# Performance work log

Hardware: AMD Instinct MI355X
Metric: run time of the kernel (lower is better)

## Reference

```python
import jax, jax.numpy as jnp
import numpy as np

HS = 512; L = 4; T = 128; M = 2048; FF = 2048; NH = 4; DH = HS // NH
STDV = 1.0 / float(np.sqrt(HS))


def setup_inputs() -> dict:
    key = jax.random.key(0)
    ks = iter(jax.random.split(key, 32))

    def u(shape):
        return jax.random.uniform(next(ks), shape, jnp.float32, -STDV, STDV)

    return {
        "x": jax.random.normal(next(ks), (1, T, HS), jnp.float32),
        "historical_states": jax.random.normal(next(ks), (M, L, HS), jnp.float32),
        "Wx": u((L, 3, HS, HS)), "bx": u((L, 3, HS)),
        "Wh": u((L, 3, HS, HS)), "bh": u((L, 3, HS)),
        "sa_Win": u((L, 3 * HS, HS)), "sa_bin": u((L, 3 * HS)),
        "sa_Wo": u((L, HS, HS)), "sa_bo": u((L, HS)),
        "ca_Win": u((L, 3 * HS, HS)), "ca_bin": u((L, 3 * HS)),
        "ca_Wo": u((L, HS, HS)), "ca_bo": u((L, HS)),
        "ff_W1": u((L, FF, HS)), "ff_b1": u((L, FF)),
        "ff_W2": u((L, HS, FF)), "ff_b2": u((L, HS)),
        "ln_g": u((L, 3, HS)), "ln_b": u((L, 3, HS)),
    }


def _layer_norm(v, g, b):
    m = v.mean(-1, keepdims=True)
    var = ((v - m) ** 2).mean(-1, keepdims=True)
    return (v - m) / jnp.sqrt(var + 1e-5) * g + b


def _forward(x, historical_states, Wx, bx, Wh, bh, sa_Win, sa_bin, sa_Wo, sa_bo,
             ca_Win, ca_bin, ca_Wo, ca_bo, ff_W1, ff_b1, ff_W2, ff_b2, ln_g, ln_b):
    n_layers, _, hs, _ = Wx.shape
    # Cross-attn K/V over the static historical memory are time-invariant: precompute once.
    Wk = ca_Win[:, hs:2 * hs, :]; bk = ca_bin[:, hs:2 * hs]
    Wv = ca_Win[:, 2 * hs:, :]; bv = ca_bin[:, 2 * hs:]
    K = (jnp.einsum('mle,lfe->lmf', historical_states, Wk) + bk[:, None, :]).reshape(n_layers, -1, NH, DH)
    V = (jnp.einsum('mle,lfe->lmf', historical_states, Wv) + bv[:, None, :]).reshape(n_layers, -1, NH, DH)
    scale = 1.0 / jnp.sqrt(jnp.asarray(DH, x.dtype))

    def decoder(i, f):
        # post-norm TransformerDecoderLayer, tgt length 1, eval mode (no dropout).
        # Self-attn over a single position: softmax of one logit == 1 -> out = Wo @ (Wv_self f + bv_self) + bo.
        v_sa = sa_Win[i, 2 * hs:] @ f + sa_bin[i, 2 * hs:]
        sa = sa_Wo[i] @ v_sa + sa_bo[i]
        x1 = _layer_norm(f + sa, ln_g[i, 0], ln_b[i, 0])
        q = (ca_Win[i, :hs] @ x1 + ca_bin[i, :hs]).reshape(NH, DH)
        att = jax.nn.softmax(jnp.einsum('hd,mhd->hm', q, K[i]) * scale, axis=-1)
        ctx = jnp.einsum('hm,mhd->hd', att, V[i]).reshape(hs)
        x2 = _layer_norm(x1 + ca_Wo[i] @ ctx + ca_bo[i], ln_g[i, 1], ln_b[i, 1])
        ff = ff_W2[i] @ jax.nn.relu(ff_W1[i] @ x2 + ff_b1[i]) + ff_b2[i]
        return _layer_norm(x2 + ff, ln_g[i, 2], ln_b[i, 2])

    def step(carry, x_t):
        h_prev, c_prev = carry  # (L, HS) each; batch is structurally 1
        xin = x_t
        h_new = []; c_new = []
        for i in range(n_layers):
            z = (jnp.einsum('gij,j->gi', Wx[i], xin) + bx[i]
                 + jnp.einsum('gij,j->gi', Wh[i], h_prev[i]) + bh[i])  # (3, HS)
            i_t = jax.nn.sigmoid(z[0]); f0 = jax.nn.sigmoid(z[1]); g_t = jnp.tanh(z[2])
            f_t = jax.nn.sigmoid(c_prev[i] - decoder(i, f0))
            c_i = f_t * c_prev[i] + i_t * g_t
            xin = jnp.tanh(c_i)
            h_new.append(xin); c_new.append(c_i)
        h = jnp.stack(h_new); c = jnp.stack(c_new)
        return (h, c), h[-1]

    h0 = jnp.zeros((n_layers, hs), x.dtype)
    c0 = jnp.zeros((n_layers, hs), x.dtype)
    (h_T, c_T), hidden = jax.lax.scan(step, (h0, c0), x[0])  # hidden: (T, HS)
    return hidden[None], h_T[:, None, :], c_T[:, None, :]


def reference(x, historical_states, Wx, bx, Wh, bh, sa_Win, sa_bin, sa_Wo, sa_bo,
              ca_Win, ca_bin, ca_Wo, ca_bo, ff_W1, ff_b1, ff_W2, ff_b2, ln_g, ln_b):
    return _forward(x, historical_states, Wx, bx, Wh, bh, sa_Win, sa_bin, sa_Wo, sa_bo,
                    ca_Win, ca_bin, ca_Wo, ca_bo, ff_W1, ff_b1, ff_W2, ff_b2, ln_g, ln_b)
```

## Files before the change

### kernel.cpp

```cpp
#include <hip/hip_runtime.h>

#define HS   512
#define LNUM 4
#define TT   128
#define MMEM 2048
#define FFD  2048
#define NB   256
#define NT   512
#define INV512 (1.0f/512.0f)
#define QSCALE 0.08838834764831845f

typedef unsigned short ushortt;

constexpr size_t KHALF = (size_t)LNUM*MMEM*HS/2;
constexpr size_t HHALF = (size_t)LNUM*HS*HS/2;
constexpr size_t FHALF = (size_t)LNUM*FFD*HS/2;
constexpr size_t OFF_KBF    = 0;
constexpr size_t OFF_VBF    = OFF_KBF    + KHALF;
constexpr size_t OFF_WCOMBBF= OFF_VBF    + KHALF;
constexpr size_t OFF_WQP    = OFF_WCOMBBF+ HHALF;
constexpr size_t OFF_W2P    = OFF_WQP    + HHALF;
constexpr size_t OFF_FFW1BF = OFF_W2P    + FHALF;
constexpr size_t OFF_CAWOBF = OFF_FFW1BF + FHALF;
constexpr size_t OFF_CSA    = OFF_CAWOBF + HHALF;
constexpr size_t OFF_SQ     = OFF_CSA    + (size_t)LNUM*HS;
constexpr size_t OFF_CBQ    = OFF_SQ     + (size_t)LNUM*HS;
constexpr size_t OFF_STATE = OFF_CBQ   + (size_t)LNUM*HS;
constexpr size_t OFF_H     = OFF_STATE;
constexpr size_t OFF_C     = OFF_H     + 2*LNUM*HS;
constexpr size_t OFF_XING  = OFF_C     + 2*LNUM*HS;
constexpr size_t OFF_Z1    = OFF_XING  + HS;
constexpr size_t OFF_Z02   = OFF_Z1    + HS;
constexpr size_t OFF_T2G   = OFF_Z02   + 2*HS;
constexpr size_t OFF_YP    = OFF_T2G   + HS;
constexpr size_t OFF_Y2P   = OFF_YP    + 4*HS;
constexpr size_t OFF_CTXP  = OFF_Y2P   + 8*HS;
constexpr size_t OFF_DENS  = OFF_CTXP  + 8*HS;
constexpr size_t OFF_S1S   = OFF_DENS  + 128;
constexpr size_t OFF_S2S   = OFF_S1S   + 64;
constexpr size_t OFF_J1    = OFF_S2S   + 64;
constexpr size_t OFF_J2    = OFF_J1    + 65*32;
constexpr size_t OFF_FLAGS = OFF_J2    + 128*32;
constexpr size_t WS_TOTAL  = OFF_FLAGS + (size_t)NB*32;

__device__ __forceinline__ float wred(float v) {
#pragma unroll
  for (int m = 32; m; m >>= 1) v += __shfl_xor(v, m);
  return v;
}
__device__ __forceinline__ float sigm(float x) { return 1.0f/(1.0f+__expf(-x)); }
__device__ __forceinline__ ushortt f2bf(float f) {
  unsigned u = __float_as_uint(f);
  return (ushortt)((u + 0x7fffu + ((u >> 16) & 1u)) >> 16);
}
__device__ __forceinline__ float bflo(unsigned v){ return __uint_as_float(v << 16); }
__device__ __forceinline__ float bfhi(unsigned v){ return __uint_as_float(v & 0xffff0000u); }
__device__ __forceinline__ void ld8bfp(const ushortt* p, unsigned* d) {
  uint4 v = *(const uint4*)p;
  d[0] = v.x; d[1] = v.y; d[2] = v.z; d[3] = v.w;
}
__device__ __forceinline__ void ld8f(const float* p, float* d) {
  float4 a = *(const float4*)p, b = *(const float4*)(p + 4);
  d[0]=a.x; d[1]=a.y; d[2]=a.z; d[3]=a.w; d[4]=b.x; d[5]=b.y; d[6]=b.z; d[7]=b.w;
}

__device__ __forceinline__ float ald(const float* p) {
  return __hip_atomic_load(p, __ATOMIC_RELAXED, __HIP_MEMORY_SCOPE_AGENT);
}
__device__ __forceinline__ void ast(float* p, float v) {
  __hip_atomic_store(p, v, __ATOMIC_RELAXED, __HIP_MEMORY_SCOPE_AGENT);
}
__device__ __forceinline__ unsigned aldu(const unsigned* p) {
  return __hip_atomic_load(p, __ATOMIC_RELAXED, __HIP_MEMORY_SCOPE_AGENT);
}
__device__ __forceinline__ void astu(unsigned* p, unsigned v) {
  __hip_atomic_store(p, v, __ATOMIC_RELAXED, __HIP_MEMORY_SCOPE_AGENT);
}

template <class F>
__device__ __forceinline__ void barrier_pf(unsigned* flags, unsigned g, F&& pf) {
  asm volatile("s_waitcnt vmcnt(0)" ::: "memory");
  __syncthreads();
  if (threadIdx.x == 0) astu(flags + (size_t)blockIdx.x*32, g);
  pf();
  if (threadIdx.x < NB) {
    const unsigned* f = flags + (size_t)threadIdx.x*32;
    while ((int)(aldu(f) - g) < 0) __builtin_amdgcn_s_sleep(2);
  }
  __syncthreads();
}
__device__ __forceinline__ void jflag(unsigned* J, int id, unsigned val) {
  asm volatile("s_waitcnt vmcnt(0)" ::: "memory");
  __syncthreads();
  if (threadIdx.x == 0) astu(J + (size_t)id*32, val);
}
template <class F>
__device__ __forceinline__ void jwait_pf(unsigned* J, int n, unsigned val, F&& pf) {
  pf();
  if (threadIdx.x < n) {
    const unsigned* f = J + (size_t)threadIdx.x*32;
    while ((int)(aldu(f) - val) < 0) __builtin_amdgcn_s_sleep(1);
  }
  __syncthreads();
}
__device__ __forceinline__ void slotred32(const float* slots, float* sh, int o,
                                          int w, int lane) {
  if (w == 0) {
    float a = (lane < 32) ? ald(slots + lane*2) : ald(slots + (lane-32)*2 + 1);
#pragma unroll
    for (int m = 16; m; m >>= 1) a += __shfl_xor(a, m);
    if (lane == 0)  sh[o]   = a;
    if (lane == 32) sh[o+1] = a;
  }
}


__global__ __launch_bounds__(256) void kv_gemm(
    const float* __restrict__ hist, const float* __restrict__ caWin,
    const float* __restrict__ caBin, ushortt* __restrict__ out, int koff, int vt) {
  __shared__ float As[16][64];
  __shared__ float Bs[16][64];
  const int l = blockIdx.z, m0 = blockIdx.x*64, f0 = blockIdx.y*64;
  const int tid = threadIdx.x, tm = tid >> 4, tf = tid & 15;
  float acc[4][4] = {};
  for (int e0 = 0; e0 < HS; e0 += 16) {
#pragma unroll
    for (int it = 0; it < 4; ++it) {
      int idx = tid + it*256, k = idx & 15, mm = idx >> 4;
      As[k][mm] = hist[((size_t)(m0+mm)*LNUM + l)*HS + e0 + k];
      Bs[k][mm] = caWin[((size_t)l*(3*HS) + koff + f0 + mm)*HS + e0 + k];
    }
    __syncthreads();
#pragma unroll
    for (int k = 0; k < 16; ++k) {
      float a[4], b[4];
#pragma unroll
      for (int xx = 0; xx < 4; ++xx) { a[xx] = As[k][tm*4+xx]; b[xx] = Bs[k][tf*4+xx]; }
#pragma unroll
      for (int xx = 0; xx < 4; ++xx)
#pragma unroll
        for (int y = 0; y < 4; ++y) acc[xx][y] += a[xx]*b[y];
    }
    __syncthreads();
  }
#pragma unroll
  for (int xx = 0; xx < 4; ++xx)
#pragma unroll
    for (int y = 0; y < 4; ++y) {
      int m = m0 + tm*4 + xx, f = f0 + tf*4 + y;
      ushortt v = f2bf(acc[xx][y] + caBin[l*(3*HS) + koff + f]);
      if (vt) out[(size_t)l*MMEM*HS + (size_t)f*MMEM + m] = v;
      else    out[((size_t)l*MMEM + m)*HS + f] = v;
    }
}

__global__ __launch_bounds__(256) void wcomb_gemm(
    const float* __restrict__ saWo, const float* __restrict__ saWin,
    ushortt* __restrict__ wcomb) {
  __shared__ float As[16][64];
  __shared__ float Bs[16][64];
  const int l = blockIdx.z, f0 = blockIdx.x*64, j0 = blockIdx.y*64;
  const int tid = threadIdx.x, tm = tid >> 4, tf = tid & 15;
  float acc[4][4] = {};
  for (int e0 = 0; e0 < HS; e0 += 16) {
#pragma unroll
    for (int it = 0; it < 4; ++it) {
      int idx = tid + it*256;
      { int k = idx & 15, ff = idx >> 4;
        As[k][ff] = saWo[((size_t)l*HS + f0+ff)*HS + e0 + k]; }
      { int jj = idx & 63, k = idx >> 6;
        Bs[k][jj] = saWin[((size_t)l*(3*HS) + 2*HS + e0 + k)*HS + j0 + jj]; }
    }
    __syncthreads();
#pragma unroll
    for (int k = 0; k < 16; ++k) {
      float a[4], b[4];
#pragma unroll
      for (int xx = 0; xx < 4; ++xx) { a[xx] = As[k][tm*4+xx]; b[xx] = Bs[k][tf*4+xx]; }
#pragma unroll
      for (int xx = 0; xx < 4; ++xx)
#pragma unroll
        for (int y = 0; y < 4; ++y) acc[xx][y] += a[xx]*b[y];
    }
    __syncthreads();
  }
#pragma unroll
  for (int xx = 0; xx < 4; ++xx)
#pragma unroll
    for (int y = 0; y < 4; ++y)
      wcomb[(size_t)l*HS*HS + (size_t)(f0+tm*4+xx)*HS + (j0+tf*4+y)] = f2bf(acc[xx][y]);
}

__global__ __launch_bounds__(256) void pack_wq(
    const float* __restrict__ caWin, const float* __restrict__ lnG,
    ushortt* __restrict__ wqp) {
  const int b = blockIdx.x, l = blockIdx.y;
  for (int idx = threadIdx.x; idx < 512*16; idx += 256) {
    int f = idx >> 4, r = idx & 15, j = b*16 + r;
    wqp[(((size_t)l*32 + b)*512 + f)*16 + r] =
        f2bf(caWin[((size_t)l*3*HS + f)*HS + j] * lnG[l*3*HS + j]);
  }
}

__global__ __launch_bounds__(256) void pack_w2(
    const float* __restrict__ ffW2, ushortt* __restrict__ w2p) {
  const int bid = blockIdx.x, l = blockIdx.y;
  for (int idx = threadIdx.x; idx < 512*8; idx += 256) {
    int f = idx >> 3, r = idx & 7;
    w2p[(((size_t)l*NB + bid)*512 + f)*8 + r] =
        f2bf(ffW2[((size_t)l*HS + f)*FFD + bid*8 + r]);
  }
}

__global__ __launch_bounds__(256) void bf16_copy(
    const float* __restrict__ in, ushortt* __restrict__ out, size_t n) {
  for (size_t i = (size_t)blockIdx.x*256 + threadIdx.x; i < n; i += (size_t)gridDim.x*256)
    out[i] = f2bf(in[i]);
}

__global__ __launch_bounds__(256) void csa_kernel(
    const float* __restrict__ saWo, const float* __restrict__ sabin,
    const float* __restrict__ sabo, float* __restrict__ csa) {
  const int w = threadIdx.x >> 6, lane = threadIdx.x & 63;
  const int row = blockIdx.x*4 + w;
  const int l = row >> 9, f = row & 511;
  float acc = 0;
#pragma unroll
  for (int k = 0; k < 8; ++k) {
    int e = lane + 64*k;
    acc += saWo[((size_t)l*HS + f)*HS + e] * sabin[l*(3*HS) + 2*HS + e];
  }
  acc = wred(acc);
  if (lane == 0) csa[row] = acc + sabo[l*HS + f];
}

__global__ __launch_bounds__(256) void sqcbq_kernel(
    const float* __restrict__ caWin, const float* __restrict__ caBin,
    const float* __restrict__ lnG, const float* __restrict__ lnB,
    float* __restrict__ sq, float* __restrict__ cbq) {
  const int w = threadIdx.x >> 6, lane = threadIdx.x & 63;
  const int row = blockIdx.x*4 + w;
  const int l = row >> 9, f = row & 511;
  float a1 = 0, a2 = 0;
#pragma unroll
  for (int k = 0; k < 8; ++k) {
    int e = lane + 64*k;
    float wv = caWin[((size_t)l*(3*HS) + f)*HS + e];
    a1 += wv * lnG[l*(3*HS) + e];
    a2 += wv * lnB[l*(3*HS) + e];
  }
  a1 = wred(a1); a2 = wred(a2);
  if (lane == 0) { sq[row] = a1; cbq[row] = a2 + caBin[l*(3*HS) + f]; }
}


__global__ __launch_bounds__(NT, 1) void seq_kernel(
    const float* __restrict__ x,
    const float* __restrict__ Wx,  const float* __restrict__ bx,
    const float* __restrict__ Wh,  const float* __restrict__ bh,
    const float* __restrict__ caBo,
    const float* __restrict__ ffB1,
    const float* __restrict__ ffB2,
    const float* __restrict__ lnG,  const float* __restrict__ lnB,
    float* __restrict__ ws, float* __restrict__ out) {
  const ushortt* Kb    = (const ushortt*)(ws + OFF_KBF);
  const ushortt* Vt    = (const ushortt*)(ws + OFF_VBF);
  const ushortt* Wcomb = (const ushortt*)(ws + OFF_WCOMBBF);
  const ushortt* WQP   = (const ushortt*)(ws + OFF_WQP);
  const ushortt* W2P   = (const ushortt*)(ws + OFF_W2P);
  const ushortt* F1b   = (const ushortt*)(ws + OFF_FFW1BF);
  const ushortt* CaWob = (const ushortt*)(ws + OFF_CAWOBF);
  const float* csag  = ws + OFF_CSA;
  const float* sqg   = ws + OFF_SQ;
  const float* cbqg  = ws + OFF_CBQ;
  float* hG    = ws + OFF_H;
  float* cG    = ws + OFF_C;
  float* xing  = ws + OFF_XING;
  float* z1g   = ws + OFF_Z1;
  float* z02g  = ws + OFF_Z02;
  float* t2g   = ws + OFF_T2G;
  float* Yp    = ws + OFF_YP;
  float* Y2p   = ws + OFF_Y2P;
  float* ctxP  = ws + OFF_CTXP;
  float* denS  = ws + OFF_DENS;
  float* s1s   = ws + OFF_S1S;
  float* s2s   = ws + OFF_S2S;
  unsigned* J1     = (unsigned*)(ws + OFF_J1);
  unsigned* J2     = (unsigned*)(ws + OFF_J2);
  unsigned* bflags = (unsigned*)(ws + OFF_FLAGS);

  __shared__ float sh_xin[HS], sh_h[HS], sh_vec[HS], sh_aux[HS];
  __shared__ float sh_q[128], sh_p[64], sh_t1[16];
  __shared__ float sh_red[24], sh_den[4];

  const int bid = blockIdx.x, tid = threadIdx.x;
  const int w = tid >> 6, lane = tid & 63;
  unsigned gen = 1;

  float    pZx[8],  pZh[8];
  float    pZx2[8], pZh2[8];
  unsigned pWc[2][4], pWq[8];
  unsigned pK[2][4],  pV[8];
  unsigned pCa[2][4];
  unsigned pF1[4], pW2[4];

  auto pfH1 = [&](int l) {
    if (bid < 64) {
      const size_t ro = (((size_t)l*3 + 1)*HS + bid*8 + w)*HS + lane*8;
      ld8f(Wx + ro, pZx);
      ld8f(Wh + ro, pZh);
    }
  };
  auto pfH2 = [&](int l) {
    if (bid < 32) {
#pragma unroll
      for (int rr = 0; rr < 2; ++rr)
        ld8bfp(Wcomb + ((size_t)l*HS + bid*16 + w*2 + rr)*HS + lane*8, pWc[rr]);
      const ushortt* q = WQP + (((size_t)l*32 + bid)*512 + tid)*16;
      ld8bfp(q,     pWq);
      ld8bfp(q + 8, pWq + 4);
    }
  };
  auto pfH3 = [&](int l) {
    if (bid >= 32 && bid < 160) {
      const int b2 = bid - 32, h = b2 >> 5, ms = b2 & 31;
#pragma unroll
      for (int rr = 0; rr < 2; ++rr)
        ld8bfp(Kb + ((size_t)l*MMEM + ms*64 + w*8 + (lane>>4) + 4*rr)*HS
                  + h*128 + (lane & 15)*8, pK[rr]);
      const ushortt* vp = Vt + (size_t)l*MMEM*HS
                        + ((size_t)h*128 + (tid & 127))*MMEM + ms*64 + (tid >> 7)*16;
      ld8bfp(vp,     pV);
      ld8bfp(vp + 8, pV + 4);
    }
  };
  auto pfZ = [&](int l) {
    if (bid < 32 || bid >= 160) {
      const int zb = (bid < 32) ? bid : bid - 128;
      const int rowid = zb*8 + w;
      const int g = (rowid < 512) ? 0 : 2;
      const int f = rowid & 511;
      const size_t ro = (((size_t)l*3 + g)*HS + f)*HS + lane*8;
      ld8f(Wx + ro, pZx2);
      ld8f(Wh + ro, pZh2);
    }
  };
  auto pfH4 = [&](int l) {
    if (bid < 32) {
#pragma unroll
      for (int rr = 0; rr < 2; ++rr)
        ld8bfp(CaWob + ((size_t)l*HS + bid*16 + w*2 + rr)*HS + lane*8, pCa[rr]);
    }
  };
  auto pfH5 = [&](int l) {
    ld8bfp(F1b + ((size_t)l*FFD + bid*8 + w)*HS + lane*8, pF1);
    ld8bfp(W2P + (((size_t)l*NB + bid)*512 + tid)*8, pW2);
  };

  auto do_update = [&](int ip, int parp, float& xn, float& cn) {
    const int j = tid;
    float t2v = ald(t2g + j);
    float z0  = ald(z02g + j);
    float z2  = ald(z02g + HS + j);
    float y2 = 0;
    {
      float yv[8];
#pragma unroll
      for (int p = 0; p < 8; ++p) yv[p] = ald(Y2p + (size_t)p*HS + j);
#pragma unroll
      for (int p = 0; p < 8; ++p) y2 += yv[p];
    }
    slotred32(s2s, sh_red, 16, w, lane);
    __syncthreads();
    float m2 = sh_red[16]*INV512;
    float r2 = rsqrtf(sh_red[17]*INV512 - m2*m2 + 1e-5f);
    float x2 = (t2v-m2)*r2*lnG[(ip*3+1)*HS+j] + lnB[(ip*3+1)*HS+j];
    float t3 = x2 + y2 + ffB2[ip*HS + j];
    float s_ = t3, q_ = t3*t3;
#pragma unroll
    for (int m = 32; m; m >>= 1) { s_ += __shfl_xor(s_, m); q_ += __shfl_xor(q_, m); }
    if (lane == 0) { sh_red[w] = s_; sh_red[8+w] = q_; }
    __syncthreads();
    if (tid == 0) {
      float a = 0, b = 0;
#pragma unroll
      for (int k = 0; k < 8; ++k) { a += sh_red[k]; b += sh_red[8+k]; }
      sh_red[0] = a; sh_red[1] = b;
    }
    __syncthreads();
    float m3 = sh_red[0]*INV512;
    float r3 = rsqrtf(sh_red[1]*INV512 - m3*m3 + 1e-5f);
    float d  = (t3-m3)*r3*lnG[(ip*3+2)*HS+j] + lnB[(ip*3+2)*HS+j];
    float cp = ald(cG + (parp*LNUM + ip)*HS + j);
    float ft = sigm(cp - d);
    float it = sigm(z0);
    float gt = tanhf(z2);
    cn = ft*cp + it*gt;
    xn = tanhf(cn);
  };

  pfH1(0); pfH2(0); pfH3(0);

  for (int s = 0; s < TT*LNUM; ++s) {
    const int t = s >> 2, i = s & 3;
    const int par = t & 1;
    const unsigned jv = (unsigned)(s + 1);
    if (bid < 64) {
      float xn = 0.f, cn = 0.f;
      if (s > 0) {
        const int ip = (s-1) & 3, tp = (s-1) >> 2, parp = tp & 1;
        if (bid == 0 || i > 0) {
          do_update(ip, parp, xn, cn);
          if (bid == 0) {
            ast(hG + ((parp^1)*LNUM + ip)*HS + tid, xn);
            ast(cG + ((parp^1)*LNUM + ip)*HS + tid, cn);
            if (ip == 3) out[tp*HS + tid] = xn;
          }
        }
      }
      float xv = (i == 0) ? x[t*HS + tid] : xn;
      sh_xin[tid] = xv;
      sh_h[tid]   = ald(hG + (par*LNUM + i)*HS + tid);
      if (bid == 0) ast(xing + tid, xv);
      __syncthreads();
      const int f = bid*8 + w;
      float acc = 0;
#pragma unroll
      for (int m = 0; m < 8; ++m)
        acc += pZx[m]*sh_xin[lane*8+m] + pZh[m]*sh_h[lane*8+m];
      acc = wred(acc);
      if (lane == 0) ast(z1g + f, acc + bx[(i*3+1)*HS + f] + bh[(i*3+1)*HS + f]);
      jflag(J1, bid, jv);
    } else if (bid == 64) {
#pragma unroll
      for (int p = 0; p < 4; ++p) ast(Yp + (size_t)p*HS + tid, 0.f);
      jflag(J1, 64, jv);
    } else if (bid == 65) {
#pragma unroll
      for (int p = 0; p < 8; ++p) ast(ctxP + (size_t)p*HS + tid, 0.f);
    } else if (bid == 66) {
      jwait_pf(J1, 65, jv, [&]{});
#pragma unroll
      for (int p = 0; p < 8; ++p) ast(Y2p + (size_t)p*HS + tid, 0.f);
    }
    if (bid < 32) {
      jwait_pf(J1, 65, jv, [&]{});
      sh_vec[tid] = sigm(ald(z1g + tid));
      __syncthreads();
#pragma unroll
      for (int rr = 0; rr < 2; ++rr) {
        const int r = w*2 + rr, j = bid*16 + r;
        float acc = 0;
#pragma unroll
        for (int k = 0; k < 4; ++k) {
          unsigned pw = pWc[rr][k];
          acc += bflo(pw)*sh_vec[lane*8 + 2*k] + bfhi(pw)*sh_vec[lane*8 + 2*k + 1];
        }
        acc = wred(acc);
        if (lane == 0) {
          float t1v = sh_vec[j] + acc + csag[i*HS + j];
          sh_t1[r]  = t1v;
          sh_aux[r] = t1v;
        }
      }
      __syncthreads();
      {
        float yl = 0;
#pragma unroll
        for (int q = 0; q < 8; ++q) {
          unsigned pw = pWq[q];
          yl += sh_aux[2*q]*bflo(pw) + sh_aux[2*q+1]*bfhi(pw);
        }
        atomicAdd(&Yp[(size_t)(bid & 3)*HS + tid], yl);
      }
      if (w == 0 && lane < 16) {
        float v = sh_aux[lane], s_ = v, q_ = v*v;
#pragma unroll
        for (int m = 8; m; m >>= 1) { s_ += __shfl_xor(s_, m); q_ += __shfl_xor(q_, m); }
        if (lane == 0) { ast(s1s + bid*2, s_); ast(s1s + bid*2 + 1, q_); }
      }
    }
    barrier_pf(bflags, gen, [&]{ pfZ(i); pfH4(i); pfH5(i); });
    if (bid >= 32 && bid < 160) {
      const int b2 = bid - 32, h = b2 >> 5;
      slotred32(s1s, sh_red, 18, w, lane);
      __syncthreads();
      if (tid < 128) {
        float m1 = sh_red[18]*INV512;
        float r1 = rsqrtf(sh_red[19]*INV512 - m1*m1 + 1e-5f);
        int f = h*128 + tid;
        float Ysum = 0;
#pragma unroll
        for (int p = 0; p < 4; ++p) Ysum += ald(Yp + (size_t)p*HS + f);
        sh_q[tid] = r1*(Ysum - m1*sqg[i*HS + f]) + cbqg[i*HS + f];
      }
      __syncthreads();
#pragma unroll
      for (int rr = 0; rr < 2; ++rr) {
        float sc = 0;
#pragma unroll
        for (int k = 0; k < 4; ++k) {
          unsigned pw = pK[rr][k];
          sc += bflo(pw)*sh_q[(lane & 15)*8 + 2*k] + bfhi(pw)*sh_q[(lane & 15)*8 + 2*k + 1];
        }
#pragma unroll
        for (int msk = 8; msk; msk >>= 1) sc += __shfl_xor(sc, msk);
        if ((lane & 15) == 0) sh_p[w*8 + (lane >> 4) + 4*rr] = __expf(sc * QSCALE);
      }
      __syncthreads();
      {
        const int d = tid & 127, mg = tid >> 7;
        float acc = 0;
#pragma unroll
        for (int q = 0; q < 8; ++q) {
          unsigned pw = pV[q];
          acc += sh_p[mg*16 + 2*q]*bflo(pw) + sh_p[mg*16 + 2*q + 1]*bfhi(pw);
        }
        atomicAdd(&ctxP[(size_t)((b2 & 1)*4 + mg)*HS + h*128 + d], acc);
      }
      if (w == 0) {
        float v = wred(sh_p[lane]);
        if (lane == 0) ast(denS + h*32 + (b2 & 31), v);
      }
      jflag(J2, b2, jv);
    } else {
      const int zb = (bid < 32) ? bid : bid - 128;
      if (bid >= 160) {
        sh_xin[tid] = ald(xing + tid);
        sh_h[tid]   = ald(hG + (par*LNUM + i)*HS + tid);
      }
      __syncthreads();
      const int rowid = zb*8 + w;
      const int g = (rowid < 512) ? 0 : 2;
      const int f = rowid & 511;
      float acc = 0;
#pragma unroll
      for (int m = 0; m < 8; ++m)
        acc += pZx2[m]*sh_xin[lane*8+m] + pZh2[m]*sh_h[lane*8+m];
      acc = wred(acc);
      if (lane == 0) ast(z02g + (g ? HS : 0) + f, acc + bx[(i*3+g)*HS + f] + bh[(i*3+g)*HS + f]);
      if (bid < 32) {
        jwait_pf(J2, 128, jv, [&]{});
        slotred32(s1s, sh_red, 18, w, lane);
        if (w >= 4) {
          float v = (lane < 32) ? ald(denS + (w-4)*32 + lane) : 0.f;
#pragma unroll
          for (int m = 16; m; m >>= 1) v += __shfl_xor(v, m);
          if (lane == 0) sh_den[w-4] = v;
        }
        __syncthreads();
        const float m1 = sh_red[18]*INV512;
        const float r1 = rsqrtf(sh_red[19]*INV512 - m1*m1 + 1e-5f);
        {
          float c = 0;
#pragma unroll
          for (int p = 0; p < 8; ++p) c += ald(ctxP + (size_t)p*HS + tid);
          sh_vec[tid] = c / sh_den[tid >> 7];
        }
        __syncthreads();
#pragma unroll
        for (int rr = 0; rr < 2; ++rr) {
          const int r = w*2 + rr, j = bid*16 + r;
          float a2 = 0;
#pragma unroll
          for (int k = 0; k < 4; ++k) {
            unsigned pw = pCa[rr][k];
            a2 += bflo(pw)*sh_vec[lane*8 + 2*k] + bfhi(pw)*sh_vec[lane*8 + 2*k + 1];
          }
          a2 = wred(a2);
          if (lane == 0) {
            float x1 = (sh_t1[r]-m1)*r1*lnG[(i*3)*HS + j] + lnB[(i*3)*HS + j];
            float t2v = x1 + a2 + caBo[i*HS + j];
            ast(t2g + j, t2v);
            sh_aux[r] = t2v;
          }
        }
        __syncthreads();
        if (w == 0 && lane < 16) {
          float v = sh_aux[lane], s_ = v, q_ = v*v;
#pragma unroll
          for (int m = 8; m; m >>= 1) { s_ += __shfl_xor(s_, m); q_ += __shfl_xor(q_, m); }
          if (lane == 0) { ast(s2s + bid*2, s_); ast(s2s + bid*2 + 1, q_); }
        }
      }
    }
    barrier_pf(bflags, gen+1, [&]{ const int nl = (s+1) & 3; pfH1(nl); pfH2(nl); pfH3(nl); });
    {
      slotred32(s2s, sh_red, 16, w, lane);
      __syncthreads();
      const float m2 = sh_red[16]*INV512;
      const float r2 = rsqrtf(sh_red[17]*INV512 - m2*m2 + 1e-5f);
      sh_vec[tid] = (ald(t2g + tid)-m2)*r2*lnG[(i*3+1)*HS + tid] + lnB[(i*3+1)*HS + tid];
      __syncthreads();
      const int kk = bid*8 + w;
      float acc = 0;
#pragma unroll
      for (int k = 0; k < 4; ++k) {
        unsigned pw = pF1[k];
        acc += bflo(pw)*sh_vec[lane*8 + 2*k] + bfhi(pw)*sh_vec[lane*8 + 2*k + 1];
      }
      acc = wred(acc);
      if (lane == 0) sh_aux[w] = fmaxf(acc + ffB1[i*FFD + kk], 0.f);
      __syncthreads();
      float yl = 0;
#pragma unroll
      for (int q = 0; q < 4; ++q) {
        unsigned pw = pW2[q];
        yl += sh_aux[2*q]*bflo(pw) + sh_aux[2*q+1]*bfhi(pw);
      }
      atomicAdd(&Y2p[(size_t)(bid & 7)*HS + tid], yl);
    }
    barrier_pf(bflags, gen+2, [&]{});
    gen += 3;
  }

  if (bid == 0) {
    float xn, cn;
    do_update(3, 1, xn, cn);
    out[127*HS + tid] = xn;
    out[TT*HS + 3*HS + tid] = xn;
    out[TT*HS + LNUM*HS + 3*HS + tid] = cn;
#pragma unroll
    for (int ii = 0; ii < 3; ++ii) {
      out[TT*HS + ii*HS + tid]            = ald(hG + (0*LNUM + ii)*HS + tid);
      out[TT*HS + LNUM*HS + ii*HS + tid]  = ald(cG + (0*LNUM + ii)*HS + tid);
    }
  }
}

extern "C" void kernel_launch(void* const* d_in, const int* in_sizes, int n_in,
                              void* d_out, int out_size, void* d_ws, size_t ws_size,
                              hipStream_t stream) {
  const float* x      = (const float*)d_in[0];
  const float* hist   = (const float*)d_in[1];
  const float* Wx     = (const float*)d_in[2];
  const float* bx     = (const float*)d_in[3];
  const float* Wh     = (const float*)d_in[4];
  const float* bh     = (const float*)d_in[5];
  const float* saWin  = (const float*)d_in[6];
  const float* saBin  = (const float*)d_in[7];
  const float* saWo   = (const float*)d_in[8];
  const float* saBo   = (const float*)d_in[9];
  const float* caWin  = (const float*)d_in[10];
  const float* caBin  = (const float*)d_in[11];
  const float* caWo   = (const float*)d_in[12];
  const float* caBo   = (const float*)d_in[13];
  const float* ffW1   = (const float*)d_in[14];
  const float* ffB1   = (const float*)d_in[15];
  const float* ffW2   = (const float*)d_in[16];
  const float* ffB2   = (const float*)d_in[17];
  const float* lnG    = (const float*)d_in[18];
  const float* lnB    = (const float*)d_in[19];
  float* ws  = (float*)d_ws;
  float* out = (float*)d_out;

  hipMemsetAsync((char*)d_ws + OFF_STATE*sizeof(float), 0,
                 (WS_TOTAL - OFF_STATE)*sizeof(float), stream);

  kv_gemm<<<dim3(MMEM/64, HS/64, LNUM), 256, 0, stream>>>(
      hist, caWin, caBin, (ushortt*)(ws + OFF_KBF), HS, 0);
  kv_gemm<<<dim3(MMEM/64, HS/64, LNUM), 256, 0, stream>>>(
      hist, caWin, caBin, (ushortt*)(ws + OFF_VBF), 2*HS, 1);
  wcomb_gemm<<<dim3(HS/64, HS/64, LNUM), 256, 0, stream>>>(
      saWo, saWin, (ushortt*)(ws + OFF_WCOMBBF));
  csa_kernel<<<(LNUM*HS)/4, 256, 0, stream>>>(saWo, saBin, saBo, ws + OFF_CSA);
  pack_wq<<<dim3(32, LNUM), 256, 0, stream>>>(caWin, lnG, (ushortt*)(ws + OFF_WQP));
  sqcbq_kernel<<<(LNUM*HS)/4, 256, 0, stream>>>(caWin, caBin, lnG, lnB, ws + OFF_SQ, ws + OFF_CBQ);
  pack_w2<<<dim3(NB, LNUM), 256, 0, stream>>>(ffW2, (ushortt*)(ws + OFF_W2P));
  bf16_copy<<<2048, 256, 0, stream>>>(ffW1, (ushortt*)(ws + OFF_FFW1BF), (size_t)LNUM*FFD*HS);
  bf16_copy<<<1024, 256, 0, stream>>>(caWo, (ushortt*)(ws + OFF_CAWOBF), (size_t)LNUM*HS*HS);

  seq_kernel<<<NB, NT, 0, stream>>>(x, Wx, bx, Wh, bh, caBo,
                                    ffB1, ffB2, lnG, lnB, ws, out);
}
```

Baseline: 11.09 ms.

## Move z0/z2 gate GEMV to idle blocks, bf16 LSTM weights, drop atomics

Wx and Wh are converted to bf16 in the workspace so the LSTM gate GEMVs read half the bytes. The z0/z2 gate rows move from blocks 0-31 and 160-255 onto blocks 64-191, which wait on a new per-step xing flag, and z02 is double-buffered by step parity. Attention partials (Yp, ctxP) now go to per-block slots with no atomics, and readers reduce them in shared memory. The FFN accumulator is spread over 64 slots and the H2/H3 prefetches move to the last barrier. The aim is to take the gate GEMV off the critical cross-attention chain and cut atomic contention, at the cost of more slot reads and a new flag protocol.

New measurement: 21.63 ms. +95.2%, slower.

```diff
diff --git a/kernel.cpp b/kernel.cpp
--- a/kernel.cpp
+++ b/kernel.cpp
@@ -15,6 +15,7 @@
 constexpr size_t KHALF = (size_t)LNUM*MMEM*HS/2;
 constexpr size_t HHALF = (size_t)LNUM*HS*HS/2;
 constexpr size_t FHALF = (size_t)LNUM*FFD*HS/2;
+constexpr size_t GHALF = (size_t)LNUM*3*HS*HS/2;
 constexpr size_t OFF_KBF    = 0;
 constexpr size_t OFF_VBF    = OFF_KBF    + KHALF;
 constexpr size_t OFF_WCOMBBF= OFF_VBF    + KHALF;
@@ -22,7 +23,9 @@
 constexpr size_t OFF_W2P    = OFF_WQP    + HHALF;
 constexpr size_t OFF_FFW1BF = OFF_W2P    + FHALF;
 constexpr size_t OFF_CAWOBF = OFF_FFW1BF + FHALF;
-constexpr size_t OFF_CSA    = OFF_CAWOBF + HHALF;
+constexpr size_t OFF_WXBF   = OFF_CAWOBF + HHALF;
+constexpr size_t OFF_WHBF   = OFF_WXBF   + GHALF;
+constexpr size_t OFF_CSA    = OFF_WHBF   + GHALF;
 constexpr size_t OFF_SQ     = OFF_CSA    + (size_t)LNUM*HS;
 constexpr size_t OFF_CBQ    = OFF_SQ     + (size_t)LNUM*HS;
 constexpr size_t OFF_STATE = OFF_CBQ   + (size_t)LNUM*HS;
@@ -31,16 +34,17 @@
 constexpr size_t OFF_XING  = OFF_C     + 2*LNUM*HS;
 constexpr size_t OFF_Z1    = OFF_XING  + HS;
 constexpr size_t OFF_Z02   = OFF_Z1    + HS;
-constexpr size_t OFF_T2G   = OFF_Z02   + 2*HS;
+constexpr size_t OFF_T2G   = OFF_Z02   + 2*2*HS;
 constexpr size_t OFF_YP    = OFF_T2G   + HS;
-constexpr size_t OFF_Y2P   = OFF_YP    + 4*HS;
-constexpr size_t OFF_CTXP  = OFF_Y2P   + 8*HS;
-constexpr size_t OFF_DENS  = OFF_CTXP  + 8*HS;
+constexpr size_t OFF_Y2P   = OFF_YP    + 32*HS;
+constexpr size_t OFF_CTXP  = OFF_Y2P   + 64*HS;
+constexpr size_t OFF_DENS  = OFF_CTXP  + 128*128;
 constexpr size_t OFF_S1S   = OFF_DENS  + 128;
 constexpr size_t OFF_S2S   = OFF_S1S   + 64;
 constexpr size_t OFF_J1    = OFF_S2S   + 64;
-constexpr size_t OFF_J2    = OFF_J1    + 65*32;
-constexpr size_t OFF_FLAGS = OFF_J2    + 128*32;
+constexpr size_t OFF_J2    = OFF_J1    + 64*32;
+constexpr size_t OFF_XFL   = OFF_J2    + 128*32;
+constexpr size_t OFF_FLAGS = OFF_XFL   + 4*32;
 constexpr size_t WS_TOTAL  = OFF_FLAGS + (size_t)NB*32;
 
 __device__ __forceinline__ float wred(float v) {
@@ -58,10 +62,6 @@
 __device__ __forceinline__ void ld8bfp(const ushortt* p, unsigned* d) {
   uint4 v = *(const uint4*)p;
   d[0] = v.x; d[1] = v.y; d[2] = v.z; d[3] = v.w;
-}
-__device__ __forceinline__ void ld8f(const float* p, float* d) {
-  float4 a = *(const float4*)p, b = *(const float4*)(p + 4);
-  d[0]=a.x; d[1]=a.y; d[2]=a.z; d[3]=a.w; d[4]=b.x; d[5]=b.y; d[6]=b.z; d[7]=b.w;
 }
 
 __device__ __forceinline__ float ald(const float* p) {
@@ -94,9 +94,7 @@
   __syncthreads();
   if (threadIdx.x == 0) astu(J + (size_t)id*32, val);
 }
-template <class F>
-__device__ __forceinline__ void jwait_pf(unsigned* J, int n, unsigned val, F&& pf) {
-  pf();
+__device__ __forceinline__ void jwait(unsigned* J, int n, unsigned val) {
   if (threadIdx.x < n) {
     const unsigned* f = J + (size_t)threadIdx.x*32;
     while ((int)(aldu(f) - val) < 0) __builtin_amdgcn_s_sleep(1);
@@ -256,8 +254,7 @@
 
 __global__ __launch_bounds__(NT, 1) void seq_kernel(
     const float* __restrict__ x,
-    const float* __restrict__ Wx,  const float* __restrict__ bx,
-    const float* __restrict__ Wh,  const float* __restrict__ bh,
+    const float* __restrict__ bx, const float* __restrict__ bh,
     const float* __restrict__ caBo,
     const float* __restrict__ ffB1,
     const float* __restrict__ ffB2,
@@ -270,6 +267,8 @@
   const ushortt* W2P   = (const ushortt*)(ws + OFF_W2P);
   const ushortt* F1b   = (const ushortt*)(ws + OFF_FFW1BF);
   const ushortt* CaWob = (const ushortt*)(ws + OFF_CAWOBF);
+  const ushortt* WXb   = (const ushortt*)(ws + OFF_WXBF);
+  const ushortt* WHb   = (const ushortt*)(ws + OFF_WHBF);
   const float* csag  = ws + OFF_CSA;
   const float* sqg   = ws + OFF_SQ;
   const float* cbqg  = ws + OFF_CBQ;
@@ -287,6 +286,7 @@
   float* s2s   = ws + OFF_S2S;
   unsigned* J1     = (unsigned*)(ws + OFF_J1);
   unsigned* J2     = (unsigned*)(ws + OFF_J2);
+  unsigned* xfl    = (unsigned*)(ws + OFF_XFL);
   unsigned* bflags = (unsigned*)(ws + OFF_FLAGS);
 
   __shared__ float sh_xin[HS], sh_h[HS], sh_vec[HS], sh_aux[HS];
@@ -295,10 +295,11 @@
 
   const int bid = blockIdx.x, tid = threadIdx.x;
   const int w = tid >> 6, lane = tid & 63;
+  const int g4 = tid >> 7, dd = tid & 127;
   unsigned gen = 1;
 
-  float    pZx[8],  pZh[8];
-  float    pZx2[8], pZh2[8];
+  unsigned pZx[4],  pZh[4];
+  unsigned pZx2[4], pZh2[4];
   unsigned pWc[2][4], pWq[8];
   unsigned pK[2][4],  pV[8];
   unsigned pCa[2][4];
@@ -307,8 +308,17 @@
   auto pfH1 = [&](int l) {
     if (bid < 64) {
       const size_t ro = (((size_t)l*3 + 1)*HS + bid*8 + w)*HS + lane*8;
-      ld8f(Wx + ro, pZx);
-      ld8f(Wh + ro, pZh);
+      ld8bfp(WXb + ro, pZx);
+      ld8bfp(WHb + ro, pZh);
+    }
+  };
+  auto pfZ02 = [&](int l) {
+    if (bid >= 64 && bid < 192) {
+      const int zb = bid - 64, rowid = zb*8 + w;
+      const int g = (rowid < 512) ? 0 : 2, f = rowid & 511;
+      const size_t ro = (((size_t)l*3 + g)*HS + f)*HS + lane*8;
+      ld8bfp(WXb + ro, pZx2);
+      ld8bfp(WHb + ro, pZh2);
     }
   };
   auto pfH2 = [&](int l) {
@@ -329,20 +339,9 @@
         ld8bfp(Kb + ((size_t)l*MMEM + ms*64 + w*8 + (lane>>4) + 4*rr)*HS
                   + h*128 + (lane & 15)*8, pK[rr]);
       const ushortt* vp = Vt + (size_t)l*MMEM*HS
-                        + ((size_t)h*128 + (tid & 127))*MMEM + ms*64 + (tid >> 7)*16;
+                        + ((size_t)h*128 + dd)*MMEM + ms*64 + g4*16;
       ld8bfp(vp,     pV);
       ld8bfp(vp + 8, pV + 4);
-    }
-  };
-  auto pfZ = [&](int l) {
-    if (bid < 32 || bid >= 160) {
-      const int zb = (bid < 32) ? bid : bid - 128;
-      const int rowid = zb*8 + w;
-      const int g = (rowid < 512) ? 0 : 2;
-      const int f = rowid & 511;
-      const size_t ro = (((size_t)l*3 + g)*HS + f)*HS + lane*8;
-      ld8f(Wx + ro, pZx2);
-      ld8f(Wh + ro, pZh2);
     }
   };
   auto pfH4 = [&](int l) {
@@ -357,18 +356,21 @@
     ld8bfp(W2P + (((size_t)l*NB + bid)*512 + tid)*8, pW2);
   };
 
-  auto do_update = [&](int ip, int parp, float& xn, float& cn) {
+  auto do_update = [&](int ip, int parp, int pz, float& xn, float& cn) {
     const int j = tid;
     float t2v = ald(t2g + j);
-    float z0  = ald(z02g + j);
-    float z2  = ald(z02g + HS + j);
+    float z0  = ald(z02g + pz*1024 + j);
+    float z2  = ald(z02g + pz*1024 + HS + j);
     float y2 = 0;
     {
-      float yv[8];
-#pragma unroll
-      for (int p = 0; p < 8; ++p) yv[p] = ald(Y2p + (size_t)p*HS + j);
-#pragma unroll
-      for (int p = 0; p < 8; ++p) y2 += yv[p];
+      float yv[16];
+#pragma unroll
+      for (int c = 0; c < 64; c += 16) {
+#pragma unroll
+        for (int p = 0; p < 16; ++p) yv[p] = ald(Y2p + (size_t)(c+p)*HS + j);
+#pragma unroll
+        for (int p = 0; p < 16; ++p) y2 += yv[p];
+      }
     }
     slotred32(s2s, sh_red, 16, w, lane);
     __syncthreads();
@@ -399,18 +401,19 @@
     xn = tanhf(cn);
   };
 
-  pfH1(0); pfH2(0); pfH3(0);
+  pfH1(0); pfZ02(0); pfH2(0); pfH3(0);
 
   for (int s = 0; s < TT*LNUM; ++s) {
     const int t = s >> 2, i = s & 3;
     const int par = t & 1;
+    const int pz = s & 1;
     const unsigned jv = (unsigned)(s + 1);
     if (bid < 64) {
       float xn = 0.f, cn = 0.f;
       if (s > 0) {
         const int ip = (s-1) & 3, tp = (s-1) >> 2, parp = tp & 1;
         if (bid == 0 || i > 0) {
-          do_update(ip, parp, xn, cn);
+          do_update(ip, parp, (s-1) & 1, xn, cn);
           if (bid == 0) {
             ast(hG + ((parp^1)*LNUM + ip)*HS + tid, xn);
             ast(cG + ((parp^1)*LNUM + ip)*HS + tid, cn);
@@ -423,28 +426,53 @@
       sh_h[tid]   = ald(hG + (par*LNUM + i)*HS + tid);
       if (bid == 0) ast(xing + tid, xv);
       __syncthreads();
+      if (bid == 0) {
+        asm volatile("s_waitcnt vmcnt(0)" ::: "memory");
+        __syncthreads();
+        if (tid < 4) astu(xfl + (size_t)tid*32, jv);
+      }
       const int f = bid*8 + w;
       float acc = 0;
 #pragma unroll
-      for (int m = 0; m < 8; ++m)
-        acc += pZx[m]*sh_xin[lane*8+m] + pZh[m]*sh_h[lane*8+m];
+      for (int k = 0; k < 4; ++k) {
+        unsigned px = pZx[k], ph = pZh[k];
+        acc += bflo(px)*sh_xin[lane*8 + 2*k] + bfhi(px)*sh_xin[lane*8 + 2*k + 1]
+             + bflo(ph)*sh_h[lane*8 + 2*k]  + bfhi(ph)*sh_h[lane*8 + 2*k + 1];
+      }
       acc = wred(acc);
       if (lane == 0) ast(z1g + f, acc + bx[(i*3+1)*HS + f] + bh[(i*3+1)*HS + f]);
       jflag(J1, bid, jv);
-    } else if (bid == 64) {
-#pragma unroll
-      for (int p = 0; p < 4; ++p) ast(Yp + (size_t)p*HS + tid, 0.f);
-      jflag(J1, 64, jv);
-    } else if (bid == 65) {
-#pragma unroll
-      for (int p = 0; p < 8; ++p) ast(ctxP + (size_t)p*HS + tid, 0.f);
-    } else if (bid == 66) {
-      jwait_pf(J1, 65, jv, [&]{});
-#pragma unroll
-      for (int p = 0; p < 8; ++p) ast(Y2p + (size_t)p*HS + tid, 0.f);
+    } else if (bid < 192) {
+      const int zb = bid - 64;
+      float xv;
+      if (i == 0) xv = x[t*HS + tid];
+      else {
+        if (tid == 0) {
+          const unsigned* f = xfl + (size_t)(bid & 3)*32;
+          while ((int)(aldu(f) - jv) < 0) __builtin_amdgcn_s_sleep(1);
+        }
+        __syncthreads();
+        xv = ald(xing + tid);
+      }
+      sh_xin[tid] = xv;
+      sh_h[tid]   = ald(hG + (par*LNUM + i)*HS + tid);
+      __syncthreads();
+      const int rowid = zb*8 + w;
+      const int g = (rowid < 512) ? 0 : 2, f = rowid & 511;
+      float acc = 0;
+#pragma unroll
+      for (int k = 0; k < 4; ++k) {
+        unsigned px = pZx2[k], ph = pZh2[k];
+        acc += bflo(px)*sh_xin[lane*8 + 2*k] + bfhi(px)*sh_xin[lane*8 + 2*k + 1]
+             + bflo(ph)*sh_h[lane*8 + 2*k]  + bfhi(ph)*sh_h[lane*8 + 2*k + 1];
+      }
+      acc = wred(acc);
+      if (lane == 0)
+        ast(z02g + pz*1024 + (g ? HS : 0) + f,
+            acc + bx[(i*3+g)*HS + f] + bh[(i*3+g)*HS + f]);
     }
     if (bid < 32) {
-      jwait_pf(J1, 65, jv, [&]{});
+      jwait(J1, 64, jv);
       sh_vec[tid] = sigm(ald(z1g + tid));
       __syncthreads();
 #pragma unroll
@@ -471,7 +499,7 @@
           unsigned pw = pWq[q];
           yl += sh_aux[2*q]*bflo(pw) + sh_aux[2*q+1]*bfhi(pw);
         }
-        atomicAdd(&Yp[(size_t)(bid & 3)*HS + tid], yl);
+        ast(Yp + (size_t)bid*HS + tid, yl);
       }
       if (w == 0 && lane < 16) {
         float v = sh_aux[lane], s_ = v, q_ = v*v;
@@ -480,18 +508,25 @@
         if (lane == 0) { ast(s1s + bid*2, s_); ast(s1s + bid*2 + 1, q_); }
       }
     }
-    barrier_pf(bflags, gen, [&]{ pfZ(i); pfH4(i); pfH5(i); });
+    barrier_pf(bflags, gen, [&]{ pfH4(i); pfH5(i); });
     if (bid >= 32 && bid < 160) {
       const int b2 = bid - 32, h = b2 >> 5;
       slotred32(s1s, sh_red, 18, w, lane);
+      {
+        float part = 0;
+        float yv[8];
+#pragma unroll
+        for (int p = 0; p < 8; ++p) yv[p] = ald(Yp + (size_t)(g4*8+p)*HS + h*128 + dd);
+#pragma unroll
+        for (int p = 0; p < 8; ++p) part += yv[p];
+        sh_vec[tid] = part;
+      }
       __syncthreads();
       if (tid < 128) {
+        float Ysum = sh_vec[tid] + sh_vec[128+tid] + sh_vec[256+tid] + sh_vec[384+tid];
         float m1 = sh_red[18]*INV512;
         float r1 = rsqrtf(sh_red[19]*INV512 - m1*m1 + 1e-5f);
         int f = h*128 + tid;
-        float Ysum = 0;
-#pragma unroll
-        for (int p = 0; p < 4; ++p) Ysum += ald(Yp + (size_t)p*HS + f);
         sh_q[tid] = r1*(Ysum - m1*sqg[i*HS + f]) + cbqg[i*HS + f];
       }
       __syncthreads();
@@ -509,82 +544,79 @@
       }
       __syncthreads();
       {
-        const int d = tid & 127, mg = tid >> 7;
         float acc = 0;
 #pragma unroll
         for (int q = 0; q < 8; ++q) {
           unsigned pw = pV[q];
-          acc += sh_p[mg*16 + 2*q]*bflo(pw) + sh_p[mg*16 + 2*q + 1]*bfhi(pw);
-        }
-        atomicAdd(&ctxP[(size_t)((b2 & 1)*4 + mg)*HS + h*128 + d], acc);
+          acc += sh_p[g4*16 + 2*q]*bflo(pw) + sh_p[g4*16 + 2*q + 1]*bfhi(pw);
+        }
+        sh_vec[tid] = acc;
       }
       if (w == 0) {
         float v = wred(sh_p[lane]);
-        if (lane == 0) ast(denS + h*32 + (b2 & 31), v);
+        if (lane == 0) ast(denS + b2, v);
+      }
+      __syncthreads();
+      if (tid < 128) {
+        float tot = sh_vec[tid] + sh_vec[128+tid] + sh_vec[256+tid] + sh_vec[384+tid];
+        ast(ctxP + (size_t)b2*128 + tid, tot);
       }
       jflag(J2, b2, jv);
-    } else {
-      const int zb = (bid < 32) ? bid : bid - 128;
-      if (bid >= 160) {
-        sh_xin[tid] = ald(xing + tid);
-        sh_h[tid]   = ald(hG + (par*LNUM + i)*HS + tid);
-      }
-      __syncthreads();
-      const int rowid = zb*8 + w;
-      const int g = (rowid < 512) ? 0 : 2;
-      const int f = rowid & 511;
-      float acc = 0;
-#pragma unroll
-      for (int m = 0; m < 8; ++m)
-        acc += pZx2[m]*sh_xin[lane*8+m] + pZh2[m]*sh_h[lane*8+m];
-      acc = wred(acc);
-      if (lane == 0) ast(z02g + (g ? HS : 0) + f, acc + bx[(i*3+g)*HS + f] + bh[(i*3+g)*HS + f]);
-      if (bid < 32) {
-        jwait_pf(J2, 128, jv, [&]{});
-        slotred32(s1s, sh_red, 18, w, lane);
-        if (w >= 4) {
-          float v = (lane < 32) ? ald(denS + (w-4)*32 + lane) : 0.f;
-#pragma unroll
-          for (int m = 16; m; m >>= 1) v += __shfl_xor(v, m);
-          if (lane == 0) sh_den[w-4] = v;
-        }
-        __syncthreads();
-        const float m1 = sh_red[18]*INV512;
-        const float r1 = rsqrtf(sh_red[19]*INV512 - m1*m1 + 1e-5f);
-        {
-          float c = 0;
-#pragma unroll
-          for (int p = 0; p < 8; ++p) c += ald(ctxP + (size_t)p*HS + tid);
-          sh_vec[tid] = c / sh_den[tid >> 7];
-        }
-        __syncthreads();
-#pragma unroll
-        for (int rr = 0; rr < 2; ++rr) {
-          const int r = w*2 + rr, j = bid*16 + r;
-          float a2 = 0;
-#pragma unroll
-          for (int k = 0; k < 4; ++k) {
-            unsigned pw = pCa[rr][k];
-            a2 += bflo(pw)*sh_vec[lane*8 + 2*k] + bfhi(pw)*sh_vec[lane*8 + 2*k + 1];
-          }
-          a2 = wred(a2);
-          if (lane == 0) {
-            float x1 = (sh_t1[r]-m1)*r1*lnG[(i*3)*HS + j] + lnB[(i*3)*HS + j];
-            float t2v = x1 + a2 + caBo[i*HS + j];
-            ast(t2g + j, t2v);
-            sh_aux[r] = t2v;
-          }
-        }
-        __syncthreads();
-        if (w == 0 && lane < 16) {
-          float v = sh_aux[lane], s_ = v, q_ = v*v;
-#pragma unroll
-          for (int m = 8; m; m >>= 1) { s_ += __shfl_xor(s_, m); q_ += __shfl_xor(q_, m); }
-          if (lane == 0) { ast(s2s + bid*2, s_); ast(s2s + bid*2 + 1, q_); }
-        }
-      }
-    }
-    barrier_pf(bflags, gen+1, [&]{ const int nl = (s+1) & 3; pfH1(nl); pfH2(nl); pfH3(nl); });
+    } else if (bid < 32) {
+      jwait(J2, 128, jv);
+      slotred32(s1s, sh_red, 18, w, lane);
+      if (w >= 4) {
+        float v = (lane < 32) ? ald(denS + (w-4)*32 + lane) : 0.f;
+#pragma unroll
+        for (int m = 16; m; m >>= 1) v += __shfl_xor(v, m);
+        if (lane == 0) sh_den[w-4] = v;
+      }
+      __syncthreads();
+      const float m1 = sh_red[18]*INV512;
+      const float r1 = rsqrtf(sh_red[19]*INV512 - m1*m1 + 1e-5f);
+      {
+        const int hh = tid >> 7;
+        float c0 = 0;
+        float cv[16];
+#pragma unroll
+        for (int c = 0; c < 32; c += 16) {
+#pragma unroll
+          for (int p = 0; p < 16; ++p)
+            cv[p] = ald(ctxP + (size_t)(hh*32 + c + p)*128 + dd);
+#pragma unroll
+          for (int p = 0; p < 16; ++p) c0 += cv[p];
+        }
+        sh_vec[tid] = c0 / sh_den[hh];
+      }
+      __syncthreads();
+#pragma unroll
+      for (int rr = 0; rr < 2; ++rr) {
+        const int r = w*2 + rr, j = bid*16 + r;
+        float a2 = 0;
+#pragma unroll
+        for (int k = 0; k < 4; ++k) {
+          unsigned pw = pCa[rr][k];
+          a2 += bflo(pw)*sh_vec[lane*8 + 2*k] + bfhi(pw)*sh_vec[lane*8 + 2*k + 1];
+        }
+        a2 = wred(a2);
+        if (lane == 0) {
+          float x1 = (sh_t1[r]-m1)*r1*lnG[(i*3)*HS + j] + lnB[(i*3)*HS + j];
+          float t2v = x1 + a2 + caBo[i*HS + j];
+          ast(t2g + j, t2v);
+          sh_aux[r] = t2v;
+        }
+      }
+      __syncthreads();
+      if (w == 0 && lane < 16) {
+        float v = sh_aux[lane], s_ = v, q_ = v*v;
+#pragma unroll
+        for (int m = 8; m; m >>= 1) { s_ += __shfl_xor(s_, m); q_ += __shfl_xor(q_, m); }
+        if (lane == 0) { ast(s2s + bid*2, s_); ast(s2s + bid*2 + 1, q_); }
+      }
+    } else if (bid >= 160 && bid < 224) {
+      ast(Y2p + (size_t)(bid-160)*HS + tid, 0.f);
+    }
+    barrier_pf(bflags, gen+1, [&]{ const int nl = (s+1) & 3; pfH1(nl); pfZ02(nl); });
     {
       slotred32(s2s, sh_red, 16, w, lane);
       __syncthreads();
@@ -608,15 +640,15 @@
         unsigned pw = pW2[q];
         yl += sh_aux[2*q]*bflo(pw) + sh_aux[2*q+1]*bfhi(pw);
       }
-      atomicAdd(&Y2p[(size_t)(bid & 7)*HS + tid], yl);
-    }
-    barrier_pf(bflags, gen+2, [&]{});
+      atomicAdd(&Y2p[(size_t)(bid & 63)*HS + tid], yl);
+    }
+    barrier_pf(bflags, gen+2, [&]{ const int nl = (s+1) & 3; pfH2(nl); pfH3(nl); });
     gen += 3;
   }
 
   if (bid == 0) {
     float xn, cn;
-    do_update(3, 1, xn, cn);
+    do_update(3, 1, 1, xn, cn);
     out[127*HS + tid] = xn;
     out[TT*HS + 3*HS + tid] = xn;
     out[TT*HS + LNUM*HS + 3*HS + tid] = cn;
@@ -669,7 +701,9 @@
   pack_w2<<<dim3(NB, LNUM), 256, 0, stream>>>(ffW2, (ushortt*)(ws + OFF_W2P));
   bf16_copy<<<2048, 256, 0, stream>>>(ffW1, (ushortt*)(ws + OFF_FFW1BF), (size_t)LNUM*FFD*HS);
   bf16_copy<<<1024, 256, 0, stream>>>(caWo, (ushortt*)(ws + OFF_CAWOBF), (size_t)LNUM*HS*HS);
-
-  seq_kernel<<<NB, NT, 0, stream>>>(x, Wx, bx, Wh, bh, caBo,
+  bf16_copy<<<2048, 256, 0, stream>>>(Wx, (ushortt*)(ws + OFF_WXBF), (size_t)LNUM*3*HS*HS);
+  bf16_copy<<<2048, 256, 0, stream>>>(Wh, (ushortt*)(ws + OFF_WHBF), (size_t)LNUM*3*HS*HS);
+
+  seq_kernel<<<NB, NT, 0, stream>>>(x, bx, bh, caBo,
                                     ffB1, ffB2, lnG, lnB, ws, out);
 }
```
